# Kernel optimization log

Hardware: AMD Instinct MI355X
Metric: run time of the kernel (lower is better)

## Reference

```python
import jax, jax.numpy as jnp
import numpy as np

N_TOKENS = 16384
HIDDEN = 4096
N_EXPERTS = 64


def setup_inputs() -> dict:
    key = jax.random.key(0)
    k1, k2 = jax.random.split(key)
    hidden_states = jax.random.normal(k1, (N_TOKENS, HIDDEN), dtype=jnp.float32)
    # nn.Linear(hidden, 3*num_experts, bias=False): weight shape [3E, H]
    W_qkv = jax.random.normal(k2, (3 * N_EXPERTS, HIDDEN), dtype=jnp.float32) * (HIDDEN ** -0.5)
    return {"hidden_states": hidden_states, "W_qkv": W_qkv}


def reference(hidden_states, W_qkv):
    # fused QKV projection: [N, 3E]
    mix = hidden_states @ W_qkv.T
    q, k, v = jnp.split(mix, 3, axis=-1)  # each [N, E]
    q = q.astype(jnp.float32)
    k = k.astype(jnp.float32)
    v = v.astype(jnp.float32)
    # per-token outer product: [N, E, E]
    attn = jnp.einsum("ne,nf->nef", q, k)
    attn = jax.nn.softmax(attn, axis=-1)
    # weighted sum over keys: [N, E]
    router_output = jnp.einsum("nef,nf->ne", attn, v)
    return router_output
```

## Files before the change

### kernel.cpp

```cpp
#include <hip/hip_runtime.h>
#include <hip/hip_fp16.h>
#include <stdint.h>

#define NTOK 16384
#define HID 4096
#define NE 64
#define NQKV 192
#define TM 64
#define BK 64
#define NCHUNK (HID / BK)

typedef _Float16 half8_t __attribute__((ext_vector_type(8)));
typedef _Float16 half4_t __attribute__((ext_vector_type(4)));
typedef float f32x4 __attribute__((ext_vector_type(4)));

#if __has_builtin(__builtin_amdgcn_exp2f)
#define EXP2F(x) __builtin_amdgcn_exp2f(x)
#else
#define EXP2F(x) exp2f(x)
#endif

__global__ void wconvert_kernel(const float* __restrict__ W, _Float16* __restrict__ W16) {
    int i = (blockIdx.x * blockDim.x + threadIdx.x) * 8;
    f32x4 a = *(const f32x4*)(W + i);
    f32x4 b = *(const f32x4*)(W + i + 4);
    half8_t h;
    h[0] = (_Float16)a[0]; h[1] = (_Float16)a[1]; h[2] = (_Float16)a[2]; h[3] = (_Float16)a[3];
    h[4] = (_Float16)b[0]; h[5] = (_Float16)b[1]; h[6] = (_Float16)b[2]; h[7] = (_Float16)b[3];
    *(half8_t*)(W16 + i) = h;
}

__global__ __launch_bounds__(256, 1) void fused_kernel(const float* __restrict__ X,
                                                       const _Float16* __restrict__ W16,
                                                       float* __restrict__ out) {
    __shared__ __align__(16) _Float16 As[2][TM * BK];
    __shared__ __align__(16) _Float16 Bs[2][NQKV * BK];
    __shared__ __align__(16) float mixS[TM][NQKV + 4];

    const int tid  = threadIdx.x;
    const int lane = tid & 63;
    const int wid  = tid >> 6;
    const int tok0 = blockIdx.x * TM;

    const int arow0 = tid >> 4;
    const int acol  = (tid & 15) * 4;
    const int aphys = ((tid & 15) >> 1) ^ (arow0 & 7);
    const int adst0 = arow0 * 64 + aphys * 8 + (tid & 1) * 4;
    const float* abase = X + (size_t)(tok0 + arow0) * HID + acol;

    f32x4 acc[12] = {};

    auto stage = [&](int buf, int kc) {
        const float* ap = abase + kc * BK;
        #pragma unroll
        for (int i = 0; i < 4; ++i) {
            f32x4 f = *(const f32x4*)(ap + (size_t)i * 16 * HID);
            half4_t h;
            h[0] = (_Float16)f[0]; h[1] = (_Float16)f[1];
            h[2] = (_Float16)f[2]; h[3] = (_Float16)f[3];
            *(half4_t*)&As[buf][adst0 + i * 1024] = h;
        }
        #pragma unroll
        for (int i = 0; i < 6; ++i) {
            int o  = i * 4096 + wid * 1024 + lane * 16;
            int r  = o >> 7;
            int cp = (o >> 4) & 7;
            int cl = cp ^ (r & 7);
            const _Float16* src = W16 + (size_t)r * HID + kc * BK + cl * 8;
            char* dst = (char*)(&Bs[buf][0]) + i * 4096 + wid * 1024;
            __builtin_amdgcn_global_load_lds(
                (const __attribute__((address_space(1))) uint32_t*)(uintptr_t)(const void*)src,
                (__attribute__((address_space(3))) uint32_t*)(uintptr_t)(void*)dst,
                16, 0, 0);
        }
    };

    auto compute = [&](int buf) {
        const int arow = wid * 16 + (lane & 15);
        #pragma unroll
        for (int kk = 0; kk < 2; ++kk) {
            const int acl = kk * 4 + (lane >> 4);
            half8_t av = *(half8_t*)&As[buf][arow * BK + ((acl ^ (arow & 7)) * 8)];
            #pragma unroll
            for (int j = 0; j < 12; ++j) {
                const int brow = j * 16 + (lane & 15);
                half8_t bv = *(half8_t*)&Bs[buf][brow * BK + ((acl ^ (brow & 7)) * 8)];
                acc[j] = __builtin_amdgcn_mfma_f32_16x16x32_f16(av, bv, acc[j], 0, 0, 0);
            }
        }
    };

    stage(0, 0);
    __syncthreads();
    for (int t = 0; t < NCHUNK; ++t) {
        const int cur = t & 1;
        if (t + 1 < NCHUNK) stage(cur ^ 1, t + 1);
        compute(cur);
        __syncthreads();
    }

    #pragma unroll
    for (int j = 0; j < 12; ++j) {
        #pragma unroll
        for (int rg = 0; rg < 4; ++rg) {
            int row = wid * 16 + (lane >> 4) * 4 + rg;
            int col = j * 16 + (lane & 15);
            mixS[row][col] = acc[j][rg];
        }
    }
    __syncthreads();

    const float L2E = 1.44269504088896f;
    for (int tt = 0; tt < 16; ++tt) {
        const int row = wid * 16 + tt;
        float q  = mixS[row][lane];
        float kl = mixS[row][NE + lane];
        float kmax = kl, kmin = kl;
        #pragma unroll
        for (int off = 32; off >= 1; off >>= 1) {
            kmax = fmaxf(kmax, __shfl_xor(kmax, off));
            kmin = fminf(kmin, __shfl_xor(kmin, off));
        }
        float m   = (q >= 0.0f) ? q * kmax : q * kmin;
        float ql  = q * L2E;
        float nml = -m * L2E;
        float sum = 0.0f, av = 0.0f;
        #pragma unroll 4
        for (int f4 = 0; f4 < 16; ++f4) {
            f32x4 kf = *(f32x4*)&mixS[row][NE + f4 * 4];
            f32x4 vf = *(f32x4*)&mixS[row][2 * NE + f4 * 4];
            #pragma unroll
            for (int u = 0; u < 4; ++u) {
                float p = EXP2F(fmaf(ql, kf[u], nml));
                sum += p;
                av = fmaf(p, vf[u], av);
            }
        }
        out[(size_t)(tok0 + row) * NE + lane] = av / sum;
    }
}

extern "C" void kernel_launch(void* const* d_in, const int* in_sizes, int n_in,
                              void* d_out, int out_size, void* d_ws, size_t ws_size,
                              hipStream_t stream) {
    const float* X = (const float*)d_in[0];
    const float* W = (const float*)d_in[1];
    float* out = (float*)d_out;
    _Float16* W16 = (_Float16*)d_ws;

    wconvert_kernel<<<(NQKV * HID) / (256 * 8), 256, 0, stream>>>(W, W16);
    fused_kernel<<<NTOK / TM, 256, 0, stream>>>(X, W16, out);
}
```

Measured before the change: 408.7 us.

## Halve token tile and alias LDS to run two blocks per CU

Cuts the token tile from 64 to 32 rows, which doubles the grid. The four waves are rearranged into a 2x2 grid, each covering 16 rows by 96 QKV columns. The mix staging buffer now aliases the GEMM double buffers, reducing LDS use so two blocks can be resident per CU (launch bounds raised to 2). The goal is more waves in flight to hide global and LDS latency. In exchange, each token now causes twice as many reads of the fp16 weight tile.

```diff
diff --git a/kernel.cpp b/kernel.cpp
--- a/kernel.cpp
+++ b/kernel.cpp
@@ -6,7 +6,7 @@
 #define HID 4096
 #define NE 64
 #define NQKV 192
-#define TM 64
+#define TM 32
 #define BK 64
 #define NCHUNK (HID / BK)
 
@@ -30,12 +30,13 @@
     *(half8_t*)(W16 + i) = h;
 }
 
-__global__ __launch_bounds__(256, 1) void fused_kernel(const float* __restrict__ X,
+__global__ __launch_bounds__(256, 2) void fused_kernel(const float* __restrict__ X,
                                                        const _Float16* __restrict__ W16,
                                                        float* __restrict__ out) {
-    __shared__ __align__(16) _Float16 As[2][TM * BK];
-    __shared__ __align__(16) _Float16 Bs[2][NQKV * BK];
-    __shared__ __align__(16) float mixS[TM][NQKV + 4];
+    __shared__ __align__(16) char smem[57344];
+    _Float16* As = (_Float16*)smem;
+    _Float16* Bs = (_Float16*)(smem + 8192);
+    float* mixS = (float*)smem;
 
     const int tid  = threadIdx.x;
     const int lane = tid & 63;
@@ -48,17 +49,17 @@
     const int adst0 = arow0 * 64 + aphys * 8 + (tid & 1) * 4;
     const float* abase = X + (size_t)(tok0 + arow0) * HID + acol;
 
-    f32x4 acc[12] = {};
+    f32x4 acc[6] = {};
 
     auto stage = [&](int buf, int kc) {
         const float* ap = abase + kc * BK;
         #pragma unroll
-        for (int i = 0; i < 4; ++i) {
+        for (int i = 0; i < 2; ++i) {
             f32x4 f = *(const f32x4*)(ap + (size_t)i * 16 * HID);
             half4_t h;
             h[0] = (_Float16)f[0]; h[1] = (_Float16)f[1];
             h[2] = (_Float16)f[2]; h[3] = (_Float16)f[3];
-            *(half4_t*)&As[buf][adst0 + i * 1024] = h;
+            *(half4_t*)&As[buf * 2048 + adst0 + i * 1024] = h;
         }
         #pragma unroll
         for (int i = 0; i < 6; ++i) {
@@ -67,7 +68,7 @@
             int cp = (o >> 4) & 7;
             int cl = cp ^ (r & 7);
             const _Float16* src = W16 + (size_t)r * HID + kc * BK + cl * 8;
-            char* dst = (char*)(&Bs[buf][0]) + i * 4096 + wid * 1024;
+            char* dst = (char*)Bs + buf * 24576 + i * 4096 + wid * 1024;
             __builtin_amdgcn_global_load_lds(
                 (const __attribute__((address_space(1))) uint32_t*)(uintptr_t)(const void*)src,
                 (__attribute__((address_space(3))) uint32_t*)(uintptr_t)(void*)dst,
@@ -75,16 +76,19 @@
         }
     };
 
+    const int rg = wid & 1;
+    const int cg = wid >> 1;
+
     auto compute = [&](int buf) {
-        const int arow = wid * 16 + (lane & 15);
+        const int arow = rg * 16 + (lane & 15);
         #pragma unroll
         for (int kk = 0; kk < 2; ++kk) {
             const int acl = kk * 4 + (lane >> 4);
-            half8_t av = *(half8_t*)&As[buf][arow * BK + ((acl ^ (arow & 7)) * 8)];
+            half8_t av = *(half8_t*)&As[buf * 2048 + arow * BK + ((acl ^ (arow & 7)) * 8)];
             #pragma unroll
-            for (int j = 0; j < 12; ++j) {
-                const int brow = j * 16 + (lane & 15);
-                half8_t bv = *(half8_t*)&Bs[buf][brow * BK + ((acl ^ (brow & 7)) * 8)];
+            for (int j = 0; j < 6; ++j) {
+                const int brow = cg * 96 + j * 16 + (lane & 15);
+                half8_t bv = *(half8_t*)&Bs[buf * 12288 + brow * BK + ((acl ^ (brow & 7)) * 8)];
                 acc[j] = __builtin_amdgcn_mfma_f32_16x16x32_f16(av, bv, acc[j], 0, 0, 0);
             }
         }
@@ -100,21 +104,21 @@
     }
 
     #pragma unroll
-    for (int j = 0; j < 12; ++j) {
+    for (int j = 0; j < 6; ++j) {
         #pragma unroll
-        for (int rg = 0; rg < 4; ++rg) {
-            int row = wid * 16 + (lane >> 4) * 4 + rg;
-            int col = j * 16 + (lane & 15);
-            mixS[row][col] = acc[j][rg];
+        for (int r = 0; r < 4; ++r) {
+            int row = rg * 16 + (lane >> 4) * 4 + r;
+            int col = cg * 96 + j * 16 + (lane & 15);
+            mixS[row * 196 + col] = acc[j][r];
         }
     }
     __syncthreads();
 
     const float L2E = 1.44269504088896f;
-    for (int tt = 0; tt < 16; ++tt) {
-        const int row = wid * 16 + tt;
-        float q  = mixS[row][lane];
-        float kl = mixS[row][NE + lane];
+    for (int tt = 0; tt < 8; ++tt) {
+        const int row = wid * 8 + tt;
+        float q  = mixS[row * 196 + lane];
+        float kl = mixS[row * 196 + NE + lane];
         float kmax = kl, kmin = kl;
         #pragma unroll
         for (int off = 32; off >= 1; off >>= 1) {
@@ -127,8 +131,8 @@
         float sum = 0.0f, av = 0.0f;
         #pragma unroll 4
         for (int f4 = 0; f4 < 16; ++f4) {
-            f32x4 kf = *(f32x4*)&mixS[row][NE + f4 * 4];
-            f32x4 vf = *(f32x4*)&mixS[row][2 * NE + f4 * 4];
+            f32x4 kf = *(f32x4*)&mixS[row * 196 + NE + f4 * 4];
+            f32x4 vf = *(f32x4*)&mixS[row * 196 + 2 * NE + f4 * 4];
             #pragma unroll
             for (int u = 0; u < 4; ++u) {
                 float p = EXP2F(fmaf(ql, kf[u], nml));
```

Result: faster. 399.4 us (-2.3%).

## Split fused kernel into LDS-free register GEMM and separate attention kernel

Applied to the files above, without the earlier changes.

Replaces the single fused LDS-staged GEMM+softmax kernel with three kernels. The weight is pre-converted into an MFMA-fragment-ordered fp16 layout, and a one-wave-per-block GEMM loads X and W fragments directly into registers with no LDS or barriers. The mix result goes to a global workspace, and a separate attention kernel computes the softmax. This removes LDS staging and block syncs and launches 512 blocks instead of 256 for better occupancy. In exchange it adds a global round trip for the mix tensor, an extra launch, and W reads through cache by every wave.

```diff
diff --git a/kernel.cpp b/kernel.cpp
--- a/kernel.cpp
+++ b/kernel.cpp
@@ -6,12 +6,9 @@
 #define HID 4096
 #define NE 64
 #define NQKV 192
-#define TM 64
-#define BK 64
-#define NCHUNK (HID / BK)
+#define NCHUNK (HID / 64)
 
 typedef _Float16 half8_t __attribute__((ext_vector_type(8)));
-typedef _Float16 half4_t __attribute__((ext_vector_type(4)));
 typedef float f32x4 __attribute__((ext_vector_type(4)));
 
 #if __has_builtin(__builtin_amdgcn_exp2f)
@@ -20,101 +17,109 @@
 #define EXP2F(x) exp2f(x)
 #endif
 
-__global__ void wconvert_kernel(const float* __restrict__ W, _Float16* __restrict__ W16) {
-    int i = (blockIdx.x * blockDim.x + threadIdx.x) * 8;
-    f32x4 a = *(const f32x4*)(W + i);
-    f32x4 b = *(const f32x4*)(W + i + 4);
+__global__ void wconvert_kernel(const float* __restrict__ W, _Float16* __restrict__ W16r) {
+    int t = blockIdx.x * blockDim.x + threadIdx.x;
+    int col = t % NQKV;
+    int g   = t / NQKV;
+    const float* src = W + (size_t)col * HID + g * 8;
+    f32x4 a = *(const f32x4*)src;
+    f32x4 b = *(const f32x4*)(src + 4);
     half8_t h;
     h[0] = (_Float16)a[0]; h[1] = (_Float16)a[1]; h[2] = (_Float16)a[2]; h[3] = (_Float16)a[3];
     h[4] = (_Float16)b[0]; h[5] = (_Float16)b[1]; h[6] = (_Float16)b[2]; h[7] = (_Float16)b[3];
-    *(half8_t*)(W16 + i) = h;
+    *(half8_t*)(W16r + (size_t)t * 8) = h;
 }
 
-__global__ __launch_bounds__(256, 1) void fused_kernel(const float* __restrict__ X,
-                                                       const _Float16* __restrict__ W16,
-                                                       float* __restrict__ out) {
-    __shared__ __align__(16) _Float16 As[2][TM * BK];
-    __shared__ __align__(16) _Float16 Bs[2][NQKV * BK];
-    __shared__ __align__(16) float mixS[TM][NQKV + 4];
+__global__ __launch_bounds__(64) void gemm_kernel(const float* __restrict__ X,
+                                                  const _Float16* __restrict__ W16r,
+                                                  float* __restrict__ mix) {
+    const int lane = threadIdx.x;
+    const int r0 = blockIdx.x * 32;
+    const int q  = lane >> 4;
+    const int rr = lane & 15;
+
+    f32x4 acc[2][12] = {};
+    f32x4 raw[2][2][2];
+
+    const float* aptr0 = X + (size_t)(r0 + rr) * HID + q * 8;
+    const float* aptr1 = X + (size_t)(r0 + 16 + rr) * HID + q * 8;
+
+    #pragma unroll
+    for (int kk = 0; kk < 2; ++kk) {
+        raw[0][kk][0] = *(const f32x4*)(aptr0 + kk * 32);
+        raw[0][kk][1] = *(const f32x4*)(aptr0 + kk * 32 + 4);
+        raw[1][kk][0] = *(const f32x4*)(aptr1 + kk * 32);
+        raw[1][kk][1] = *(const f32x4*)(aptr1 + kk * 32 + 4);
+    }
+
+    for (int kc = 0; kc < NCHUNK; ++kc) {
+        half8_t a[2][2];
+        #pragma unroll
+        for (int rt = 0; rt < 2; ++rt)
+            #pragma unroll
+            for (int kk = 0; kk < 2; ++kk)
+                #pragma unroll
+                for (int u = 0; u < 4; ++u) {
+                    a[rt][kk][u]     = (_Float16)raw[rt][kk][0][u];
+                    a[rt][kk][u + 4] = (_Float16)raw[rt][kk][1][u];
+                }
+        if (kc + 1 < NCHUNK) {
+            const int o = (kc + 1) * 64;
+            #pragma unroll
+            for (int kk = 0; kk < 2; ++kk) {
+                raw[0][kk][0] = *(const f32x4*)(aptr0 + o + kk * 32);
+                raw[0][kk][1] = *(const f32x4*)(aptr0 + o + kk * 32 + 4);
+                raw[1][kk][0] = *(const f32x4*)(aptr1 + o + kk * 32);
+                raw[1][kk][1] = *(const f32x4*)(aptr1 + o + kk * 32 + 4);
+            }
+        }
+        #pragma unroll
+        for (int kk = 0; kk < 2; ++kk) {
+            const _Float16* bb = W16r + ((size_t)(kc * 2 + kk) * 4 + q) * 1536 + rr * 8;
+            half8_t b[12];
+            #pragma unroll
+            for (int j = 0; j < 12; ++j)
+                b[j] = *(const half8_t*)(bb + j * 128);
+            #pragma unroll
+            for (int j = 0; j < 12; ++j) {
+                acc[0][j] = __builtin_amdgcn_mfma_f32_16x16x32_f16(a[0][kk], b[j], acc[0][j], 0, 0, 0);
+                acc[1][j] = __builtin_amdgcn_mfma_f32_16x16x32_f16(a[1][kk], b[j], acc[1][j], 0, 0, 0);
+            }
+        }
+    }
+
+    #pragma unroll
+    for (int rt = 0; rt < 2; ++rt)
+        #pragma unroll
+        for (int j = 0; j < 12; ++j)
+            #pragma unroll
+            for (int rg = 0; rg < 4; ++rg)
+                mix[(size_t)(r0 + rt * 16 + q * 4 + rg) * NQKV + j * 16 + rr] = acc[rt][j][rg];
+}
+
+__global__ __launch_bounds__(256) void attn_kernel(const float* __restrict__ mix,
+                                                   float* __restrict__ out) {
+    __shared__ __align__(16) float mixS[32 * 200];
 
     const int tid  = threadIdx.x;
     const int lane = tid & 63;
     const int wid  = tid >> 6;
-    const int tok0 = blockIdx.x * TM;
-
-    const int arow0 = tid >> 4;
-    const int acol  = (tid & 15) * 4;
-    const int aphys = ((tid & 15) >> 1) ^ (arow0 & 7);
-    const int adst0 = arow0 * 64 + aphys * 8 + (tid & 1) * 4;
-    const float* abase = X + (size_t)(tok0 + arow0) * HID + acol;
-
-    f32x4 acc[12] = {};
-
-    auto stage = [&](int buf, int kc) {
-        const float* ap = abase + kc * BK;
-        #pragma unroll
-        for (int i = 0; i < 4; ++i) {
-            f32x4 f = *(const f32x4*)(ap + (size_t)i * 16 * HID);
-            half4_t h;
-            h[0] = (_Float16)f[0]; h[1] = (_Float16)f[1];
-            h[2] = (_Float16)f[2]; h[3] = (_Float16)f[3];
-            *(half4_t*)&As[buf][adst0 + i * 1024] = h;
-        }
-        #pragma unroll
-        for (int i = 0; i < 6; ++i) {
-            int o  = i * 4096 + wid * 1024 + lane * 16;
-            int r  = o >> 7;
-            int cp = (o >> 4) & 7;
-            int cl = cp ^ (r & 7);
-            const _Float16* src = W16 + (size_t)r * HID + kc * BK + cl * 8;
-            char* dst = (char*)(&Bs[buf][0]) + i * 4096 + wid * 1024;
-            __builtin_amdgcn_global_load_lds(
-                (const __attribute__((address_space(1))) uint32_t*)(uintptr_t)(const void*)src,
-                (__attribute__((address_space(3))) uint32_t*)(uintptr_t)(void*)dst,
-                16, 0, 0);
-        }
-    };
-
-    auto compute = [&](int buf) {
-        const int arow = wid * 16 + (lane & 15);
-        #pragma unroll
-        for (int kk = 0; kk < 2; ++kk) {
-            const int acl = kk * 4 + (lane >> 4);
-            half8_t av = *(half8_t*)&As[buf][arow * BK + ((acl ^ (arow & 7)) * 8)];
-            #pragma unroll
-            for (int j = 0; j < 12; ++j) {
-                const int brow = j * 16 + (lane & 15);
-                half8_t bv = *(half8_t*)&Bs[buf][brow * BK + ((acl ^ (brow & 7)) * 8)];
-                acc[j] = __builtin_amdgcn_mfma_f32_16x16x32_f16(av, bv, acc[j], 0, 0, 0);
-            }
-        }
-    };
-
-    stage(0, 0);
-    __syncthreads();
-    for (int t = 0; t < NCHUNK; ++t) {
-        const int cur = t & 1;
-        if (t + 1 < NCHUNK) stage(cur ^ 1, t + 1);
-        compute(cur);
-        __syncthreads();
-    }
+    const int tok0 = blockIdx.x * 32;
 
     #pragma unroll
-    for (int j = 0; j < 12; ++j) {
-        #pragma unroll
-        for (int rg = 0; rg < 4; ++rg) {
-            int row = wid * 16 + (lane >> 4) * 4 + rg;
-            int col = j * 16 + (lane & 15);
-            mixS[row][col] = acc[j][rg];
-        }
+    for (int p = 0; p < 6; ++p) {
+        int s = tid + p * 256;
+        int r = s / 48, g = s % 48;
+        f32x4 v = *(const f32x4*)(mix + (size_t)(tok0 + r) * NQKV + g * 4);
+        *(f32x4*)&mixS[r * 200 + g * 4] = v;
     }
     __syncthreads();
 
     const float L2E = 1.44269504088896f;
-    for (int tt = 0; tt < 16; ++tt) {
-        const int row = wid * 16 + tt;
-        float q  = mixS[row][lane];
-        float kl = mixS[row][NE + lane];
+    for (int tt = 0; tt < 8; ++tt) {
+        const int row = wid * 8 + tt;
+        float q  = mixS[row * 200 + lane];
+        float kl = mixS[row * 200 + NE + lane];
         float kmax = kl, kmin = kl;
         #pragma unroll
         for (int off = 32; off >= 1; off >>= 1) {
@@ -127,8 +132,8 @@
         float sum = 0.0f, av = 0.0f;
         #pragma unroll 4
         for (int f4 = 0; f4 < 16; ++f4) {
-            f32x4 kf = *(f32x4*)&mixS[row][NE + f4 * 4];
-            f32x4 vf = *(f32x4*)&mixS[row][2 * NE + f4 * 4];
+            f32x4 kf = *(f32x4*)&mixS[row * 200 + NE + f4 * 4];
+            f32x4 vf = *(f32x4*)&mixS[row * 200 + 2 * NE + f4 * 4];
             #pragma unroll
             for (int u = 0; u < 4; ++u) {
                 float p = EXP2F(fmaf(ql, kf[u], nml));
@@ -146,8 +151,11 @@
     const float* X = (const float*)d_in[0];
     const float* W = (const float*)d_in[1];
     float* out = (float*)d_out;
-    _Float16* W16 = (_Float16*)d_ws;
 
-    wconvert_kernel<<<(NQKV * HID) / (256 * 8), 256, 0, stream>>>(W, W16);
-    fused_kernel<<<NTOK / TM, 256, 0, stream>>>(X, W16, out);
+    _Float16* W16r = (_Float16*)d_ws;
+    float* mix = (float*)((char*)d_ws + (16u << 20));
+
+    wconvert_kernel<<<(NQKV * HID / 8) / 256, 256, 0, stream>>>(W, W16r);
+    gemm_kernel<<<NTOK / 32, 64, 0, stream>>>(X, W16r, mix);
+    attn_kernel<<<NTOK / 32, 256, 0, stream>>>(mix, out);
 }
```

Result: slower. 596.2 us (+45.9%).
